# Performance work log

Hardware: AMD Instinct MI355X
Metric: run time of the kernel (lower is better)

The kernel has to match this reference:

```python
import jax, jax.numpy as jnp
import numpy as np

NUM_GRAPHS = 64


def setup_inputs() -> dict:
    key = jax.random.key(0)
    ks = jax.random.split(key, 8)
    N, E, D_IN, D_H = 50000, 800000, 128, 256
    x = jax.random.uniform(ks[0], (N, D_IN), dtype=jnp.float32)
    edge_index = jax.random.randint(ks[1], (2, E), 0, N, dtype=jnp.int64)
    batch = jnp.sort(jax.random.randint(ks[2], (N,), 0, NUM_GRAPHS, dtype=jnp.int64))
    s = 1.0 / np.sqrt(D_IN)
    s2 = 1.0 / np.sqrt(D_H)
    W1_rel = jax.random.normal(ks[3], (D_IN, D_H), dtype=jnp.float32) * s
    W1_root = jax.random.normal(ks[4], (D_IN, D_H), dtype=jnp.float32) * s
    b1 = jnp.zeros((D_H,), jnp.float32)
    W2_rel = jax.random.normal(ks[5], (D_H, D_H), dtype=jnp.float32) * s2
    W2_root = jax.random.normal(ks[6], (D_H, D_H), dtype=jnp.float32) * s2
    b2 = jnp.zeros((D_H,), jnp.float32)
    return {"x": x, "edge_index": edge_index, "batch": batch,
            "W1_rel": W1_rel, "W1_root": W1_root, "b1": b1,
            "W2_rel": W2_rel, "W2_root": W2_root, "b2": b2}


def reference(x, edge_index, batch, W1_rel, W1_root, b1, W2_rel, W2_root, b2):
    N = x.shape[0]
    src, dst = edge_index[0], edge_index[1]

    # handcrafted features: per-label fraction of total feature mass + log(graph_size)
    graph_size = jnp.sum(x)
    handcrafted = jnp.concatenate([jnp.sum(x, axis=0) / graph_size,
                                   jnp.log(graph_size)[None]])

    def graph_conv(h, W_rel, W_root, b):
        # PyG GraphConv (aggr='add'): out_i = W_rel @ sum_{j->i} h_j + W_root @ h_i + b
        agg = jax.ops.segment_sum(h[src], dst, num_segments=N)  # [N, d]
        return agg @ W_rel + h @ W_root + b

    h = jax.nn.relu(graph_conv(x, W1_rel, W1_root, b1))
    # layers 2..num_layers share the same weights (module instance reused in original)
    for _ in range(2):
        h = jax.nn.relu(graph_conv(h, W2_rel, W2_root, b2))

    # global_mean_pool over batch ids
    counts = jax.ops.segment_sum(jnp.ones((N,), h.dtype), batch, num_segments=NUM_GRAPHS)
    pooled = jax.ops.segment_sum(h, batch, num_segments=NUM_GRAPHS)
    pooled = pooled / jnp.maximum(counts, 1.0)[:, None]
    return pooled, handcrafted
```

## Files before the change

### kernel.cpp

```cpp
#include <hip/hip_runtime.h>
#include <hip/hip_bf16.h>
#include <string.h>

#define NN 50000
#define NE 800000
#define DIN 128
#define DH 256
#define NG 64
#define PSPLIT 8

typedef short bf16x8 __attribute__((ext_vector_type(8)));
typedef float f32x4 __attribute__((ext_vector_type(4)));

__device__ __forceinline__ float bf2f(__hip_bfloat16 v) { return __bfloat162float(v); }
__device__ __forceinline__ float bfbits(unsigned int lo16) {
  unsigned int u = lo16 << 16;
  float f;
  memcpy(&f, &u, 4);
  return f;
}
__device__ __forceinline__ unsigned int packbf2(float x, float y) {
  __hip_bfloat16 bx = __float2bfloat16(x), by = __float2bfloat16(y);
  unsigned short ux, uy;
  memcpy(&ux, &bx, 2);
  memcpy(&uy, &by, 2);
  return (unsigned int)ux | ((unsigned int)uy << 16);
}

__device__ __forceinline__ float loadF(const void* p, long i, int fbf) {
  return fbf ? bf2f(((const __hip_bfloat16*)p)[i]) : ((const float*)p)[i];
}
__device__ __forceinline__ void storeF(void* p, long i, float v, int fbf) {
  if (fbf) ((__hip_bfloat16*)p)[i] = __float2bfloat16(v);
  else ((float*)p)[i] = v;
}
__device__ __forceinline__ int loadI(const void* p, long i, int i64) {
  return i64 ? (int)((const long long*)p)[i] : ((const int*)p)[i];
}

__global__ void k_detect(const void* x, const void* ei, int* flags) {
  __shared__ int s_f32sig, s_i32sig;
  if (threadIdx.x == 0) { s_f32sig = 0; s_i32sig = 0; }
  __syncthreads();
  int t = threadIdx.x;
  const unsigned short* u = (const unsigned short*)x;
  int f = 0;
  for (int i = 2 * t; i < 8192; i += 512) if (u[i] >= 0x4000) f = 1;
  const unsigned int* w = (const unsigned int*)ei;
  int g = 0;
  for (int i = 2 * t + 1; i < 8192; i += 512) if (w[i] != 0u) g = 1;
  if (f) atomicOr(&s_f32sig, 1);
  if (g) atomicOr(&s_i32sig, 1);
  __syncthreads();
  if (t == 0) { flags[0] = s_f32sig ? 0 : 1; flags[1] = s_i32sig ? 0 : 1; }
}

__global__ void k_zero(int* __restrict__ p, int n) {
  int i = blockIdx.x * blockDim.x + threadIdx.x;
  int stride = gridDim.x * blockDim.x;
  for (; i < n; i += stride) p[i] = 0;
}

__global__ void k_colsum(const void* __restrict__ x, float* __restrict__ colsum,
                         const int* __restrict__ flags) {
  int fbf = flags[0];
  int col = threadIdx.x;
  float acc = 0.f;
  for (int r = blockIdx.x; r < NN; r += gridDim.x)
    acc += loadF(x, (long)r * DIN + col, fbf);
  atomicAdd(&colsum[col], acc);
}

__global__ void k_handcrafted(const float* __restrict__ colsum, void* __restrict__ out,
                              const int* __restrict__ flags) {
  __shared__ float s[DIN];
  int fbf = flags[0];
  int t = threadIdx.x;
  s[t] = colsum[t];
  __syncthreads();
  for (int off = DIN / 2; off > 0; off >>= 1) {
    if (t < off) s[t] += s[t + off];
    __syncthreads();
  }
  float g = s[0];
  storeF(out, NG * DH + t, colsum[t] / g, fbf);
  if (t == 0) storeF(out, NG * DH + DIN, logf(g), fbf);
}

__global__ void k_convert(const void* __restrict__ x, __hip_bfloat16* __restrict__ xb,
                          const int* __restrict__ flags, int n) {
  int fbf = flags[0];
  int i = blockIdx.x * blockDim.x + threadIdx.x;
  int stride = gridDim.x * blockDim.x;
  for (; i < n; i += stride) xb[i] = __float2bfloat16(loadF(x, i, fbf));
}

__global__ void k_pack_w(const void* __restrict__ Wrel, const void* __restrict__ Wroot,
                         const void* __restrict__ bias, __hip_bfloat16* __restrict__ pack,
                         float* __restrict__ biasf, const int* __restrict__ flags, int K) {
  int fbf = flags[0];
  int KS = K >> 5;
  int total = 2 * K * DH;
  int i = blockIdx.x * blockDim.x + threadIdx.x;
  int stride = gridDim.x * blockDim.x;
  for (int p = i; p < total; p += stride) {
    int m = p / (K * DH);
    int r = p % (K * DH);
    int j = r & 7;
    int l = (r >> 3) & 63;
    int q2 = r >> 9;
    int ks = q2 % KS;
    int ct = q2 / KS;
    int kk = ks * 32 + (l >> 4) * 8 + j;
    int col = ct * 16 + (l & 15);
    const void* W = m ? Wroot : Wrel;
    pack[p] = __float2bfloat16(loadF(W, (long)kk * DH + col, fbf));
  }
  if (i < DH) biasf[i] = loadF(bias, i, fbf);
}

__global__ void k_deg(const void* __restrict__ ei, int* __restrict__ cnt,
                      const int* __restrict__ flags) {
  int i64 = flags[1];
  int e = blockIdx.x * blockDim.x + threadIdx.x;
  int stride = gridDim.x * blockDim.x;
  for (; e < NE; e += stride) {
    int d = loadI(ei, (long)NE + e, i64);
    d = min(max(d, 0), NN - 1);
    atomicAdd(&cnt[d], 1);
  }
}

#define SCAN_B 256
__global__ void k_scan1(const int* __restrict__ cnt, int* __restrict__ rowptr,
                        int* __restrict__ bsum) {
  __shared__ int s[SCAN_B];
  int b = blockIdx.x, t = threadIdx.x;
  int i = b * SCAN_B + t;
  int v = (i < NN) ? cnt[i] : 0;
  s[t] = v;
  __syncthreads();
  for (int off = 1; off < SCAN_B; off <<= 1) {
    int xv = (t >= off) ? s[t - off] : 0;
    __syncthreads();
    s[t] += xv;
    __syncthreads();
  }
  if (i < NN) rowptr[i] = s[t] - v;
  if (t == SCAN_B - 1) bsum[b] = s[t];
}

__global__ void k_scan2(int* __restrict__ bsum, int nb) {
  __shared__ int s[SCAN_B];
  int t = threadIdx.x;
  int v = (t < nb) ? bsum[t] : 0;
  s[t] = v;
  __syncthreads();
  for (int off = 1; off < SCAN_B; off <<= 1) {
    int xv = (t >= off) ? s[t - off] : 0;
    __syncthreads();
    s[t] += xv;
    __syncthreads();
  }
  if (t < nb) bsum[t] = s[t] - v;
}

__global__ void k_scan3(int* __restrict__ rowptr, const int* __restrict__ bsum) {
  int i = blockIdx.x * blockDim.x + threadIdx.x;
  int stride = gridDim.x * blockDim.x;
  for (; i < NN; i += stride) rowptr[i] += bsum[i >> 8];
  if (blockIdx.x == 0 && threadIdx.x == 0) rowptr[NN] = NE;
}

__global__ void k_fill(const void* __restrict__ ei, const int* __restrict__ rowptr,
                       int* __restrict__ cur, int* __restrict__ srcs,
                       const int* __restrict__ flags) {
  int i64 = flags[1];
  int e = blockIdx.x * blockDim.x + threadIdx.x;
  int stride = gridDim.x * blockDim.x;
  for (; e < NE; e += stride) {
    int s = loadI(ei, e, i64);
    int d = loadI(ei, (long)NE + e, i64);
    s = min(max(s, 0), NN - 1);
    d = min(max(d, 0), NN - 1);
    int p = atomicAdd(&cur[d], 1);
    srcs[rowptr[d] + p] = s;
  }
}

__global__ __launch_bounds__(256) void k_gather256(
    const int* __restrict__ rowptr, const int* __restrict__ srcs,
    const __hip_bfloat16* __restrict__ h, __hip_bfloat16* __restrict__ agg) {
  int node = blockIdx.x * 4 + (threadIdx.x >> 6);
  if (node >= NN) return;
  int lane = threadIdx.x & 63;
  int beg = rowptr[node], end = rowptr[node + 1];
  const uint2* h2 = (const uint2*)h;
  float a0 = 0.f, a1 = 0.f, a2 = 0.f, a3 = 0.f;
  int i = beg;
  for (; i + 1 < end; i += 2) {
    int s0 = srcs[i], s1 = srcs[i + 1];
    uint2 v0 = h2[(long)s0 * 64 + lane];
    uint2 v1 = h2[(long)s1 * 64 + lane];
    a0 += bfbits(v0.x & 0xffffu) + bfbits(v1.x & 0xffffu);
    a1 += bfbits(v0.x >> 16) + bfbits(v1.x >> 16);
    a2 += bfbits(v0.y & 0xffffu) + bfbits(v1.y & 0xffffu);
    a3 += bfbits(v0.y >> 16) + bfbits(v1.y >> 16);
  }
  if (i < end) {
    uint2 v0 = h2[(long)srcs[i] * 64 + lane];
    a0 += bfbits(v0.x & 0xffffu);
    a1 += bfbits(v0.x >> 16);
    a2 += bfbits(v0.y & 0xffffu);
    a3 += bfbits(v0.y >> 16);
  }
  uint2 o;
  o.x = packbf2(a0, a1);
  o.y = packbf2(a2, a3);
  ((uint2*)agg)[(long)node * 64 + lane] = o;
}

__global__ __launch_bounds__(256) void k_gather128(
    const int* __restrict__ rowptr, const int* __restrict__ srcs,
    const __hip_bfloat16* __restrict__ h, __hip_bfloat16* __restrict__ agg) {
  int node = blockIdx.x * 4 + (threadIdx.x >> 6);
  if (node >= NN) return;
  int lane = threadIdx.x & 63;
  int beg = rowptr[node], end = rowptr[node + 1];
  const unsigned int* h2 = (const unsigned int*)h;
  float a0 = 0.f, a1 = 0.f;
  int i = beg;
  for (; i + 1 < end; i += 2) {
    unsigned int v0 = h2[(long)srcs[i] * 64 + lane];
    unsigned int v1 = h2[(long)srcs[i + 1] * 64 + lane];
    a0 += bfbits(v0 & 0xffffu) + bfbits(v1 & 0xffffu);
    a1 += bfbits(v0 >> 16) + bfbits(v1 >> 16);
  }
  if (i < end) {
    unsigned int v0 = h2[(long)srcs[i] * 64 + lane];
    a0 += bfbits(v0 & 0xffffu);
    a1 += bfbits(v0 >> 16);
  }
  ((unsigned int*)agg)[(long)node * 64 + lane] = packbf2(a0, a1);
}

__global__ __launch_bounds__(256) void k_gemm(
    const __hip_bfloat16* __restrict__ A1, const __hip_bfloat16* __restrict__ A2,
    const __hip_bfloat16* __restrict__ Wpack, const float* __restrict__ bias,
    __hip_bfloat16* __restrict__ out, int K) {
  int KS = K >> 5;
  int lane = threadIdx.x & 63;
  int wave = threadIdx.x >> 6;
  int m15 = lane & 15;
  int q = lane >> 4;
  int row0 = blockIdx.x * 64;
  const short* A1s = (const short*)A1;
  const short* A2s = (const short*)A2;
  const short* Wp = (const short*)Wpack;
  int wrootOfs = K * DH;
  f32x4 acc[4][4] = {};
  for (int ks = 0; ks < KS; ++ks) {
    int kofs = ks * 32 + q * 8;
    bf16x8 a1[4], a2[4], b1[4], b2[4];
#pragma unroll
    for (int mt = 0; mt < 4; ++mt) {
      int r = row0 + mt * 16 + m15;
      if (r > NN - 1) r = NN - 1;
      a1[mt] = *(const bf16x8*)(A1s + r * K + kofs);
      a2[mt] = *(const bf16x8*)(A2s + r * K + kofs);
    }
#pragma unroll
    for (int ct = 0; ct < 4; ++ct) {
      int gct = wave * 4 + ct;
      const short* base = Wp + ((gct * KS + ks) * 64 + lane) * 8;
      b1[ct] = *(const bf16x8*)(base);
      b2[ct] = *(const bf16x8*)(base + wrootOfs);
    }
#pragma unroll
    for (int mt = 0; mt < 4; ++mt)
#pragma unroll
      for (int ct = 0; ct < 4; ++ct) {
        acc[mt][ct] = __builtin_amdgcn_mfma_f32_16x16x32_bf16(a1[mt], b1[ct], acc[mt][ct], 0, 0, 0);
        acc[mt][ct] = __builtin_amdgcn_mfma_f32_16x16x32_bf16(a2[mt], b2[ct], acc[mt][ct], 0, 0, 0);
      }
  }
#pragma unroll
  for (int mt = 0; mt < 4; ++mt)
#pragma unroll
    for (int ct = 0; ct < 4; ++ct) {
      int col = wave * 64 + ct * 16 + m15;
      float bv = bias[col];
#pragma unroll
      for (int r = 0; r < 4; ++r) {
        int row = row0 + mt * 16 + q * 4 + r;
        if (row < NN) {
          float v = acc[mt][ct][r] + bv;
          out[row * DH + col] = __float2bfloat16(fmaxf(v, 0.f));
        }
      }
    }
}

__global__ void k_bounds(const void* __restrict__ batch, int* __restrict__ gstart,
                         int* __restrict__ gend, const int* __restrict__ flags) {
  int i64 = flags[1];
  int n = blockIdx.x * blockDim.x + threadIdx.x;
  if (n >= NN) return;
  int b = min(max(loadI(batch, n, i64), 0), NG - 1);
  int bp = (n == 0) ? -1 : min(max(loadI(batch, n - 1, i64), 0), NG - 1);
  if (b != bp) gstart[b] = n;
  int bn = (n == NN - 1) ? -1 : min(max(loadI(batch, n + 1, i64), 0), NG - 1);
  if (b != bn) gend[b] = n + 1;
}

__global__ void k_poolpart(const int* __restrict__ gstart, const int* __restrict__ gend,
                           const __hip_bfloat16* __restrict__ h, float* __restrict__ pooled) {
  int g = blockIdx.x;
  int p = blockIdx.y;
  int j = threadIdx.x;
  int s = gstart[g], e = gend[g];
  int len = e - s;
  if (len <= 0) return;
  int chunk = (len + PSPLIT - 1) / PSPLIT;
  int rs = s + p * chunk;
  int re = min(rs + chunk, e);
  if (rs >= re) return;
  const unsigned int* h2 = (const unsigned int*)h;
  float a0 = 0.f, a1 = 0.f;
  for (int r = rs; r < re; ++r) {
    unsigned int v = h2[(long)r * 128 + j];
    a0 += bfbits(v & 0xffffu);
    a1 += bfbits(v >> 16);
  }
  atomicAdd(&pooled[g * DH + 2 * j], a0);
  atomicAdd(&pooled[g * DH + 2 * j + 1], a1);
}

__global__ void k_poolfin(const int* __restrict__ gstart, const int* __restrict__ gend,
                          const float* __restrict__ pooled, void* __restrict__ out,
                          const int* __restrict__ flags) {
  int fbf = flags[0];
  int g = blockIdx.x;
  int j = threadIdx.x;
  float cnt = fmaxf((float)(gend[g] - gstart[g]), 1.0f);
  storeF(out, (long)g * DH + j, pooled[g * DH + j] / cnt, fbf);
}

extern "C" void kernel_launch(void* const* d_in, const int* in_sizes, int n_in,
                              void* d_out, int out_size, void* d_ws, size_t ws_size,
                              hipStream_t stream) {
  const void* x = d_in[0];
  const void* ei = d_in[1];
  const void* batch = d_in[2];
  const void* W1r = d_in[3];
  const void* W1o = d_in[4];
  const void* b1 = d_in[5];
  const void* W2r = d_in[6];
  const void* W2o = d_in[7];
  const void* b2 = d_in[8];
  void* out = d_out;

  char* w = (char*)d_ws;
  auto alloc = [&](size_t bytes) -> char* {
    char* p = w;
    w += (bytes + 255) & ~(size_t)255;
    return p;
  };
  int* flags = (int*)alloc(64);
  const int zero_n = NN + NN + DIN + NG + NG + NG * DH;
  int* zreg = (int*)alloc((size_t)zero_n * 4);
  int* cnt = zreg;
  int* cur = cnt + NN;
  float* colsum = (float*)(cur + NN);
  int* gstart = (int*)(colsum + DIN);
  int* gend = gstart + NG;
  float* pooled = (float*)(gend + NG);
  int* rowptr = (int*)alloc((NN + 1) * 4);
  int* bsum = (int*)alloc(SCAN_B * 4);
  int* srcs = (int*)alloc((size_t)NE * 4);
  __hip_bfloat16* xb = (__hip_bfloat16*)alloc((size_t)NN * DIN * 2);
  __hip_bfloat16* aggb = (__hip_bfloat16*)alloc((size_t)NN * DH * 2);
  __hip_bfloat16* h = (__hip_bfloat16*)alloc((size_t)NN * DH * 2);
  __hip_bfloat16* wp1 = (__hip_bfloat16*)alloc((size_t)2 * DIN * DH * 2);
  __hip_bfloat16* wp2 = (__hip_bfloat16*)alloc((size_t)2 * DH * DH * 2);
  float* b1f = (float*)alloc(DH * 4);
  float* b2f = (float*)alloc(DH * 4);

  const int nblk = (NN + SCAN_B - 1) / SCAN_B;
  const int gemm_grid = (NN + 63) / 64;
  const int gat_grid = (NN + 3) / 4;

  k_detect<<<1, 256, 0, stream>>>(x, ei, flags);
  k_zero<<<512, 256, 0, stream>>>(zreg, zero_n);

  k_pack_w<<<64, 256, 0, stream>>>(W1r, W1o, b1, wp1, b1f, flags, DIN);
  k_pack_w<<<128, 256, 0, stream>>>(W2r, W2o, b2, wp2, b2f, flags, DH);
  k_convert<<<2048, 256, 0, stream>>>(x, xb, flags, NN * DIN);
  k_colsum<<<512, 128, 0, stream>>>(x, colsum, flags);
  k_handcrafted<<<1, 128, 0, stream>>>(colsum, out, flags);

  k_deg<<<1024, 256, 0, stream>>>(ei, cnt, flags);
  k_scan1<<<nblk, SCAN_B, 0, stream>>>(cnt, rowptr, bsum);
  k_scan2<<<1, SCAN_B, 0, stream>>>(bsum, nblk);
  k_scan3<<<256, 256, 0, stream>>>(rowptr, bsum);
  k_fill<<<1024, 256, 0, stream>>>(ei, rowptr, cur, srcs, flags);

  k_gather128<<<gat_grid, 256, 0, stream>>>(rowptr, srcs, xb, aggb);
  k_gemm<<<gemm_grid, 256, 0, stream>>>(aggb, xb, wp1, b1f, h, DIN);
  k_gather256<<<gat_grid, 256, 0, stream>>>(rowptr, srcs, h, aggb);
  k_gemm<<<gemm_grid, 256, 0, stream>>>(aggb, h, wp2, b2f, h, DH);
  k_gather256<<<gat_grid, 256, 0, stream>>>(rowptr, srcs, h, aggb);
  k_gemm<<<gemm_grid, 256, 0, stream>>>(aggb, h, wp2, b2f, h, DH);

  k_bounds<<<nblk, 256, 0, stream>>>(batch, gstart, gend, flags);
  k_poolpart<<<dim3(NG, PSPLIT), 128, 0, stream>>>(gstart, gend, h, pooled);
  k_poolfin<<<NG, DH, 0, stream>>>(gstart, gend, pooled, out, flags);
}
```

Baseline: 604.5 us.

## Fuse input conversion into column-sum, unroll gathers by four, raise pool split

Merges the fp32-to-bf16 conversion of x into the column-sum kernel, so x is read once and one launch is dropped. Unrolls both neighbor-gather loops from two to four edges per iteration, giving more loads in flight per wave, and switches their index math to 32-bit. Raises the pooling split factor from 8 to 32 for more parallelism in the partial pool. The fused prep kernel uses a 512x128 grid, which may give lower write bandwidth than the old 2048-block convert kernel.

```diff
diff --git a/kernel.cpp b/kernel.cpp
--- a/kernel.cpp
+++ b/kernel.cpp
@@ -7,7 +7,7 @@
 #define DIN 128
 #define DH 256
 #define NG 64
-#define PSPLIT 8
+#define PSPLIT 32
 
 typedef short bf16x8 __attribute__((ext_vector_type(8)));
 typedef float f32x4 __attribute__((ext_vector_type(4)));
@@ -61,13 +61,16 @@
   for (; i < n; i += stride) p[i] = 0;
 }
 
-__global__ void k_colsum(const void* __restrict__ x, float* __restrict__ colsum,
-                         const int* __restrict__ flags) {
+__global__ void k_prep(const void* __restrict__ x, __hip_bfloat16* __restrict__ xb,
+                       float* __restrict__ colsum, const int* __restrict__ flags) {
   int fbf = flags[0];
   int col = threadIdx.x;
   float acc = 0.f;
-  for (int r = blockIdx.x; r < NN; r += gridDim.x)
-    acc += loadF(x, (long)r * DIN + col, fbf);
+  for (int r = blockIdx.x; r < NN; r += gridDim.x) {
+    float v = loadF(x, (long)r * DIN + col, fbf);
+    acc += v;
+    xb[(long)r * DIN + col] = __float2bfloat16(v);
+  }
   atomicAdd(&colsum[col], acc);
 }
 
@@ -85,14 +88,6 @@
   float g = s[0];
   storeF(out, NG * DH + t, colsum[t] / g, fbf);
   if (t == 0) storeF(out, NG * DH + DIN, logf(g), fbf);
-}
-
-__global__ void k_convert(const void* __restrict__ x, __hip_bfloat16* __restrict__ xb,
-                          const int* __restrict__ flags, int n) {
-  int fbf = flags[0];
-  int i = blockIdx.x * blockDim.x + threadIdx.x;
-  int stride = gridDim.x * blockDim.x;
-  for (; i < n; i += stride) xb[i] = __float2bfloat16(loadF(x, i, fbf));
 }
 
 __global__ void k_pack_w(const void* __restrict__ Wrel, const void* __restrict__ Wroot,
@@ -198,17 +193,22 @@
   const uint2* h2 = (const uint2*)h;
   float a0 = 0.f, a1 = 0.f, a2 = 0.f, a3 = 0.f;
   int i = beg;
-  for (; i + 1 < end; i += 2) {
-    int s0 = srcs[i], s1 = srcs[i + 1];
-    uint2 v0 = h2[(long)s0 * 64 + lane];
-    uint2 v1 = h2[(long)s1 * 64 + lane];
-    a0 += bfbits(v0.x & 0xffffu) + bfbits(v1.x & 0xffffu);
-    a1 += bfbits(v0.x >> 16) + bfbits(v1.x >> 16);
-    a2 += bfbits(v0.y & 0xffffu) + bfbits(v1.y & 0xffffu);
-    a3 += bfbits(v0.y >> 16) + bfbits(v1.y >> 16);
-  }
-  if (i < end) {
-    uint2 v0 = h2[(long)srcs[i] * 64 + lane];
+  for (; i + 3 < end; i += 4) {
+    int s0 = srcs[i] * 64 + lane;
+    int s1 = srcs[i + 1] * 64 + lane;
+    int s2 = srcs[i + 2] * 64 + lane;
+    int s3 = srcs[i + 3] * 64 + lane;
+    uint2 v0 = h2[s0];
+    uint2 v1 = h2[s1];
+    uint2 v2 = h2[s2];
+    uint2 v3 = h2[s3];
+    a0 += bfbits(v0.x & 0xffffu) + bfbits(v1.x & 0xffffu) + bfbits(v2.x & 0xffffu) + bfbits(v3.x & 0xffffu);
+    a1 += bfbits(v0.x >> 16) + bfbits(v1.x >> 16) + bfbits(v2.x >> 16) + bfbits(v3.x >> 16);
+    a2 += bfbits(v0.y & 0xffffu) + bfbits(v1.y & 0xffffu) + bfbits(v2.y & 0xffffu) + bfbits(v3.y & 0xffffu);
+    a3 += bfbits(v0.y >> 16) + bfbits(v1.y >> 16) + bfbits(v2.y >> 16) + bfbits(v3.y >> 16);
+  }
+  for (; i < end; ++i) {
+    uint2 v0 = h2[srcs[i] * 64 + lane];
     a0 += bfbits(v0.x & 0xffffu);
     a1 += bfbits(v0.x >> 16);
     a2 += bfbits(v0.y & 0xffffu);
@@ -217,7 +217,7 @@
   uint2 o;
   o.x = packbf2(a0, a1);
   o.y = packbf2(a2, a3);
-  ((uint2*)agg)[(long)node * 64 + lane] = o;
+  ((uint2*)agg)[node * 64 + lane] = o;
 }
 
 __global__ __launch_bounds__(256) void k_gather128(
@@ -230,18 +230,20 @@
   const unsigned int* h2 = (const unsigned int*)h;
   float a0 = 0.f, a1 = 0.f;
   int i = beg;
-  for (; i + 1 < end; i += 2) {
-    unsigned int v0 = h2[(long)srcs[i] * 64 + lane];
-    unsigned int v1 = h2[(long)srcs[i + 1] * 64 + lane];
-    a0 += bfbits(v0 & 0xffffu) + bfbits(v1 & 0xffffu);
-    a1 += bfbits(v0 >> 16) + bfbits(v1 >> 16);
-  }
-  if (i < end) {
-    unsigned int v0 = h2[(long)srcs[i] * 64 + lane];
+  for (; i + 3 < end; i += 4) {
+    unsigned int v0 = h2[srcs[i] * 64 + lane];
+    unsigned int v1 = h2[srcs[i + 1] * 64 + lane];
+    unsigned int v2 = h2[srcs[i + 2] * 64 + lane];
+    unsigned int v3 = h2[srcs[i + 3] * 64 + lane];
+    a0 += bfbits(v0 & 0xffffu) + bfbits(v1 & 0xffffu) + bfbits(v2 & 0xffffu) + bfbits(v3 & 0xffffu);
+    a1 += bfbits(v0 >> 16) + bfbits(v1 >> 16) + bfbits(v2 >> 16) + bfbits(v3 >> 16);
+  }
+  for (; i < end; ++i) {
+    unsigned int v0 = h2[srcs[i] * 64 + lane];
     a0 += bfbits(v0 & 0xffffu);
     a1 += bfbits(v0 >> 16);
   }
-  ((unsigned int*)agg)[(long)node * 64 + lane] = packbf2(a0, a1);
+  ((unsigned int*)agg)[node * 64 + lane] = packbf2(a0, a1);
 }
 
 __global__ __launch_bounds__(256) void k_gemm(
@@ -395,8 +397,7 @@
 
   k_pack_w<<<64, 256, 0, stream>>>(W1r, W1o, b1, wp1, b1f, flags, DIN);
   k_pack_w<<<128, 256, 0, stream>>>(W2r, W2o, b2, wp2, b2f, flags, DH);
-  k_convert<<<2048, 256, 0, stream>>>(x, xb, flags, NN * DIN);
-  k_colsum<<<512, 128, 0, stream>>>(x, colsum, flags);
+  k_prep<<<512, 128, 0, stream>>>(x, xb, colsum, flags);
   k_handcrafted<<<1, 128, 0, stream>>>(colsum, out, flags);
 
   k_deg<<<1024, 256, 0, stream>>>(ei, cnt, flags);
```

After: 535.6 us. 1.13x faster.
